# Kernel tuning notes

Hardware: AMD Instinct MI355X
Metric: run time of the kernel (lower is better)

The kernel has to match this reference:

```python
import jax, jax.numpy as jnp
import numpy as np

QLEN, BSZ, D_MODEL = 2048, 4, 1024
N_HEAD, D_HEAD = 16, 64
SCALE = 1.0 / D_HEAD ** 0.5


def _rope(t, cos, sin):
    # t: [len, b, n, d_head]; cos/sin: [len, d_head//2]
    tr = t.reshape(*t.shape[:-1], D_HEAD // 2, 2)
    t_r, t_i = tr[..., 0], tr[..., 1]
    c = cos[:, None, None, :]
    s = sin[:, None, None, :]
    o_r = t_r * c - t_i * s
    o_i = t_r * s + t_i * c
    return jnp.stack([o_r, o_i], axis=-1).reshape(t.shape)


def setup_inputs() -> dict:
    key = jax.random.key(0)
    ks = jax.random.split(key, 9)
    x = jax.random.normal(ks[0], (QLEN, BSZ, D_MODEL), dtype=jnp.float32)
    # standard RoPE frequencies: theta = 10000^{-2i/d_head}
    inv_freq = 1.0 / (10000.0 ** (np.arange(0, D_HEAD, 2, dtype=np.float32) / D_HEAD))
    ang = np.arange(QLEN, dtype=np.float32)[:, None] * inv_freq[None, :]
    freqs_cos = jnp.asarray(np.cos(ang))
    freqs_sin = jnp.asarray(np.sin(ang))
    init = lambda k, sh: (jax.random.normal(k, sh, dtype=jnp.float32) * 0.02)
    H = N_HEAD * D_HEAD
    return {
        "x": x,
        "freqs_cos": freqs_cos,
        "freqs_sin": freqs_sin,
        "Wq": init(ks[1], (D_MODEL, H)), "bq": jnp.zeros((H,), jnp.float32),
        "Wk": init(ks[2], (D_MODEL, H)), "bk": jnp.zeros((H,), jnp.float32),
        "Wv": init(ks[3], (D_MODEL, H)), "bv": jnp.zeros((H,), jnp.float32),
        "Wo": init(ks[4], (H, D_MODEL)), "bo": jnp.zeros((D_MODEL,), jnp.float32),
    }


def reference(x, freqs_cos, freqs_sin, Wq, bq, Wk, bk, Wv, bv, Wo, bo):
    qlen, bsz, _ = x.shape
    q = x @ Wq + bq  # [q, b, n*d]
    k = x @ Wk + bk
    v = x @ Wv + bv
    new_mem = (k, v)
    q = q.reshape(qlen, bsz, N_HEAD, D_HEAD)
    k = k.reshape(qlen, bsz, N_HEAD, D_HEAD)
    vv = v.reshape(qlen, bsz, N_HEAD, D_HEAD)
    q = _rope(q, freqs_cos, freqs_sin)
    k = _rope(k, freqs_cos, freqs_sin)
    attn = jnp.einsum('ibnd,jbnd->ijbn', q, k) * SCALE
    p = jax.nn.softmax(attn, axis=1)
    o = jnp.einsum('ijbn,jbnd->ibnd', p, vv)
    o = o.reshape(qlen, bsz, N_HEAD * D_HEAD) @ Wo + bo
    return (o, new_mem[0], new_mem[1])
```

## Files before the change

### kernel.cpp

```cpp
#include <hip/hip_runtime.h>

typedef __attribute__((ext_vector_type(2))) float f32x2;
typedef __attribute__((ext_vector_type(4))) float f32x4;
typedef __attribute__((ext_vector_type(16))) float f32x16;
typedef __attribute__((ext_vector_type(8))) __bf16 bf16x8;
typedef __attribute__((ext_vector_type(4))) __bf16 bf16x4;
typedef __attribute__((ext_vector_type(2))) __bf16 bf16x2;
typedef __attribute__((ext_vector_type(4))) unsigned int u32x4;

#define DEVI __device__ __forceinline__

static constexpr int QLEN = 2048, BSZ = 4, DM = 1024, NH = 16, DH = 64;
static constexpr int MROWS = QLEN * BSZ;
static constexpr long OSZ  = (long)MROWS * DM;
static constexpr float SCL2E = 0.125f * 1.4426950408889634f;

DEVI void gload_lds16(const void* g, void* l) {
  __builtin_amdgcn_global_load_lds(
      (__attribute__((address_space(1))) void*)(size_t)g,
      (__attribute__((address_space(3))) void*)l, 16, 0, 0);
}

DEVI f32x16 zero16() {
  f32x16 v;
#pragma unroll
  for (int i = 0; i < 16; ++i) v[i] = 0.f;
  return v;
}

DEVI unsigned pack_bf16(float lo, float hi) {
  bf16x2 v = { (__bf16)lo, (__bf16)hi };
  return __builtin_bit_cast(unsigned, v);
}

struct f2x8 { f32x2 h[8]; };

DEVI f32x2 pk_add(f32x2 a, f32x2 b) {
  f32x2 d;
  asm("v_pk_add_f32 %0, %1, %2" : "=v"(d) : "v"(a), "v"(b));
  return d;
}

__global__ void k_f32_to_bf16(const float* __restrict__ in, __bf16* __restrict__ out, int n4) {
  int i = blockIdx.x * blockDim.x + threadIdx.x;
  int stride = gridDim.x * blockDim.x;
  for (; i < n4; i += stride) {
    const float4 v = ((const float4*)in)[i];
    bf16x4 o = { (__bf16)v.x, (__bf16)v.y, (__bf16)v.z, (__bf16)v.w };
    ((bf16x4*)out)[i] = o;
  }
}

__global__ void k_wtrans4(const float* __restrict__ W0, const float* __restrict__ W1,
                          const float* __restrict__ W2, const float* __restrict__ W3,
                          __bf16* __restrict__ WtAll) {
  __shared__ float tile[64][65];
  const int g = blockIdx.x >> 8;
  const float* W = g == 0 ? W0 : (g == 1 ? W1 : (g == 2 ? W2 : W3));
  __bf16* Wt = WtAll + (size_t)g * DM * DM;
  const int bid = blockIdx.x & 255;
  const int tk = bid >> 4;
  const int tn = bid & 15;
  const int t = threadIdx.x;
  const int r = t >> 4;
  const int c4 = (t & 15) << 2;
#pragma unroll
  for (int i = 0; i < 4; ++i) {
    const float4 v = *(const float4*)&W[(size_t)(tk * 64 + r + i * 16) * DM + tn * 64 + c4];
    tile[r + i * 16][c4 + 0] = v.x;
    tile[r + i * 16][c4 + 1] = v.y;
    tile[r + i * 16][c4 + 2] = v.z;
    tile[r + i * 16][c4 + 3] = v.w;
  }
  __syncthreads();
#pragma unroll
  for (int i = 0; i < 4; ++i) {
    const int n = r + i * 16;
    bf16x4 o = { (__bf16)tile[c4 + 0][n], (__bf16)tile[c4 + 1][n],
                 (__bf16)tile[c4 + 2][n], (__bf16)tile[c4 + 3][n] };
    *(bf16x4*)&Wt[(size_t)(tn * 64 + n) * DM + tk * 64 + c4] = o;
  }
}

__global__ __launch_bounds__(256, 4) void k_vtrans(const __bf16* __restrict__ vb,
                                                   __bf16* __restrict__ VT) {
  __shared__ __bf16 tile[128 * 72];
  const int t = threadIdx.x;
  const int bh = blockIdx.x >> 4;
  const int s0 = (blockIdx.x & 15) * 128;
  const int b = bh >> 4, h = bh & 15;

  {
    const int r = t >> 1, hh = t & 1;
    const __bf16* src = vb + (size_t)((s0 + r) * 4 + b) * DM + h * 64 + hh * 32;
    __bf16* dst = tile + r * 72 + hh * 32;
#pragma unroll
    for (int k = 0; k < 4; ++k)
      *(bf16x8*)(dst + k * 8) = *(const bf16x8*)(src + k * 8);
  }
  __syncthreads();

  const int l = t & 63;
  const int w = t >> 6;
  const int hf = l >> 5;
#pragma unroll
  for (int gi = 0; gi < 4; ++gi) {
    const int idx = w * 4 + gi;
    const int ktl = idx >> 3;
    const int fi = idx & 7;
    const int jc = fi >> 1, dh = fi & 1;
    const int d = dh * 32 + (l & 31);
    const int j8 = ktl * 64 + jc * 16 + hf * 8;
    bf16x8 pk;
#pragma unroll
    for (int jj = 0; jj < 8; ++jj) pk[jj] = tile[(j8 + jj) * 72 + d];
    const int kt_g = (blockIdx.x & 15) * 2 + ktl;
    *(bf16x8*)&VT[(size_t)(((bh * 32 + kt_g) * 8 + fi) * 64 + l) * 8] = pk;
  }
}

DEVI void gemm_tile_core(const __bf16* __restrict__ A, const __bf16* __restrict__ Bt,
                         char* Alds, char* Blds, int m0, int n0, int t,
                         f32x4 (&acc)[4][4]) {
  constexpr int K = 1024;
  const int l = t & 63;
  const int w = t >> 6;
  const int wr = w >> 1, wc = w & 1;

  int a_addr[2][4], b_addr[2][4];
#pragma unroll
  for (int s = 0; s < 2; ++s)
#pragma unroll
    for (int f = 0; f < 4; ++f) {
      const int ca = s * 64 + ((l >> 4) << 4);
      const int ra = wr * 64 + f * 16 + (l & 15);
      a_addr[s][f] = ra * 128 + (ca ^ ((ra & 7) << 4));
      const int rb = wc * 64 + f * 16 + (l & 15);
      b_addr[s][f] = rb * 128 + (ca ^ ((rb & 7) << 4));
    }

  int g_row[4], g_col[4];
#pragma unroll
  for (int i = 0; i < 4; ++i) {
    const int g = i * 256 + t;
    g_row[i] = g >> 3;
    g_col[i] = ((g & 7) ^ (g_row[i] & 7)) * 8;
  }

  for (int kt = 0; kt < K / 64; ++kt) {
#pragma unroll
    for (int i = 0; i < 4; ++i) {
      gload_lds16(A + (size_t)(m0 + g_row[i]) * K + kt * 64 + g_col[i],
                  Alds + (size_t)(i * 256 + t) * 16);
      gload_lds16(Bt + (size_t)(n0 + g_row[i]) * K + kt * 64 + g_col[i],
                  Blds + (size_t)(i * 256 + t) * 16);
    }
    __syncthreads();
#pragma unroll
    for (int s = 0; s < 2; ++s) {
      bf16x8 af[4], bfr[4];
#pragma unroll
      for (int f = 0; f < 4; ++f) {
        af[f]  = *(const bf16x8*)(Alds + a_addr[s][f]);
        bfr[f] = *(const bf16x8*)(Blds + b_addr[s][f]);
      }
      __builtin_amdgcn_s_setprio(1);
#pragma unroll
      for (int mi = 0; mi < 4; ++mi)
#pragma unroll
        for (int ni = 0; ni < 4; ++ni)
          acc[mi][ni] = __builtin_amdgcn_mfma_f32_16x16x32_bf16(af[mi], bfr[ni], acc[mi][ni], 0, 0, 0);
      __builtin_amdgcn_s_setprio(0);
    }
    __syncthreads();
  }
}

__global__ __launch_bounds__(256, 3) void k_gemm(
    const __bf16* __restrict__ A, const __bf16* __restrict__ Bt,
    const float* __restrict__ bias, float* __restrict__ Cf) {
  __shared__ alignas(16) char lds[32768];
  const int t = threadIdx.x;
  const int l = t & 63;
  const int w = t >> 6;
  const int n0 = (blockIdx.x & 7) * 128;
  const int m0 = (blockIdx.x >> 3) * 128;
  const int wr = w >> 1, wc = w & 1;

  f32x4 acc[4][4];
#pragma unroll
  for (int i = 0; i < 4; ++i)
#pragma unroll
    for (int j = 0; j < 4; ++j) acc[i][j] = (f32x4){0.f, 0.f, 0.f, 0.f};

  gemm_tile_core(A, Bt, lds, lds + 16384, m0, n0, t, acc);

  const int rowb = m0 + wr * 64 + ((l >> 4) << 2);
  const int colb = n0 + wc * 64 + (l & 15);
#pragma unroll
  for (int ni = 0; ni < 4; ++ni) {
    const float bv = bias[colb + ni * 16];
#pragma unroll
    for (int mi = 0; mi < 4; ++mi)
#pragma unroll
      for (int r = 0; r < 4; ++r)
        Cf[(size_t)(rowb + mi * 16 + r) * 1024 + colb + ni * 16] = acc[mi][ni][r] + bv;
  }
}

__global__ __launch_bounds__(256, 3) void k_gemm_qkv(
    const __bf16* __restrict__ A, const __bf16* __restrict__ Bt,
    const float* __restrict__ bq, const float* __restrict__ bk, const float* __restrict__ bv,
    const float* __restrict__ fc, const float* __restrict__ fs,
    float* __restrict__ ok, float* __restrict__ ov,
    __bf16* __restrict__ qr, __bf16* __restrict__ kr, __bf16* __restrict__ vb) {
  __shared__ alignas(16) char lds[32768];
  const int t = threadIdx.x;
  const int l = t & 63;
  const int w = t >> 6;
  const int nt = blockIdx.x % 24;
  const int n0 = nt * 128;
  const int m0 = (blockIdx.x / 24) * 128;
  const int wr = w >> 1, wc = w & 1;

  f32x4 acc[4][4];
#pragma unroll
  for (int i = 0; i < 4; ++i)
#pragma unroll
    for (int j = 0; j < 4; ++j) acc[i][j] = (f32x4){0.f, 0.f, 0.f, 0.f};

  gemm_tile_core(A, Bt, lds, lds + 16384, m0, n0, t, acc);

  const int grp = n0 >> 10;
  const int rowb = m0 + wr * 64 + ((l >> 4) << 2);
  const int colb = (n0 & 1023) + wc * 64 + (l & 15);

  if (grp == 2) {
#pragma unroll
    for (int ni = 0; ni < 4; ++ni) {
      const float bvv = bv[colb + ni * 16];
#pragma unroll
      for (int mi = 0; mi < 4; ++mi)
#pragma unroll
        for (int r = 0; r < 4; ++r) {
          const float v = acc[mi][ni][r] + bvv;
          const size_t idx = (size_t)(rowb + mi * 16 + r) * 1024 + colb + ni * 16;
          ov[idx] = v;
          vb[idx] = (__bf16)v;
        }
    }
  } else {
    const float* bias = grp == 0 ? bq : bk;
    __bf16* Rb = grp == 0 ? qr : kr;
    const float scl = grp == 0 ? SCL2E : 1.0f;
    const float sgn = (l & 1) ? 1.f : -1.f;
#pragma unroll
    for (int ni = 0; ni < 4; ++ni) {
      const int col = colb + ni * 16;
      const float bvv = bias[col];
      const int p = (col & 63) >> 1;
#pragma unroll
      for (int mi = 0; mi < 4; ++mi) {
        const int s_idx = (rowb + mi * 16) >> 2;
        const float cv = fc[s_idx * 32 + p] * scl;
        const float sv = fs[s_idx * 32 + p] * scl * sgn;
#pragma unroll
        for (int r = 0; r < 4; ++r) {
          const float v = acc[mi][ni][r] + bvv;
          if (grp == 1) ok[(size_t)(rowb + mi * 16 + r) * 1024 + col] = v;
          const float part = __shfl_xor(v, 1);
          Rb[(size_t)(rowb + mi * 16 + r) * 1024 + col] = (__bf16)(v * cv + part * sv);
        }
      }
    }
  }
}

static constexpr int FBUF9 = 16384;

__global__ __launch_bounds__(256, 4) void k_flash9(
    const __bf16* __restrict__ Q, const __bf16* __restrict__ Kr,
    const __bf16* __restrict__ VT, __bf16* __restrict__ O) {
  __shared__ alignas(16) char lds[2 * FBUF9];

  const int t = threadIdx.x, l = t & 63, w = t >> 6;
  const int hf = l >> 5;
  const int q32 = l & 31;
  const int swz = (blockIdx.x & 7) * 128 + (blockIdx.x >> 3);
  const int qt = swz & 15;
  const int bh = swz >> 4;
  const int b = bh >> 4, hd = bh & 15;

  const int qrow = qt * 128 + w * 32 + q32;

  bf16x8 qf[4];
#pragma unroll
  for (int kc = 0; kc < 4; ++kc)
    qf[kc] = *(const bf16x8*)(Q + (size_t)(qrow * 4 + b) * DM + hd * 64 + kc * 16 + hf * 8);

  f32x16 acc0 = zero16(), acc1 = zero16();
  float l_run = 0.f;

  const size_t KSTRIDE = (size_t)64 * 4 * DM;
  const size_t VSTRIDE = (size_t)512 * 8;
  const __bf16* kp0 = Kr + (size_t)((t & 31) * 4 + b) * DM + hd * 64 + (t >> 5) * 8;
  const __bf16* kp1 = kp0 + (size_t)32 * 4 * DM;
  const __bf16* vp0 = VT + ((size_t)(bh * 32) * 512 + t) * 8;
  const __bf16* vp1 = vp0 + 256 * 8;

  char* const K0 = lds;
  char* const V0 = lds + 8192;
  char* const K1 = lds + FBUF9;
  char* const V1 = K1 + 8192;

#define STAGE9(Kn, Vn)                          \
  do {                                          \
    gload_lds16(kp0, (Kn) + t * 16);            \
    gload_lds16(kp1, (Kn) + 4096 + t * 16);     \
    gload_lds16(vp0, (Vn) + t * 16);            \
    gload_lds16(vp1, (Vn) + 4096 + t * 16);     \
    kp0 += KSTRIDE; kp1 += KSTRIDE;             \
    vp0 += VSTRIDE; vp1 += VSTRIDE;             \
  } while (0)

  auto PROCESS = [&](const char* Kl, const char* Vl) {
    f32x16 s0 = zero16(), s1 = zero16();
    __builtin_amdgcn_s_setprio(1);
#pragma unroll
    for (int kc = 0; kc < 4; ++kc) {
      const bf16x8 kf0 = *(const bf16x8*)(Kl + (0 * 4 + kc) * 1024 + l * 16);
      const bf16x8 kf1 = *(const bf16x8*)(Kl + (1 * 4 + kc) * 1024 + l * 16);
      s0 = __builtin_amdgcn_mfma_f32_32x32x16_bf16(kf0, qf[kc], s0, 0, 0, 0);
      s1 = __builtin_amdgcn_mfma_f32_32x32x16_bf16(kf1, qf[kc], s1, 0, 0, 0);
    }
    __builtin_amdgcn_s_setprio(0);

    f32x16 p0, p1;
#pragma unroll
    for (int r = 0; r < 16; ++r) {
      p0[r] = __builtin_amdgcn_exp2f(s0[r]);
      p1[r] = __builtin_amdgcn_exp2f(s1[r]);
    }

    const f2x8 P0 = __builtin_bit_cast(f2x8, p0);
    const f2x8 P1 = __builtin_bit_cast(f2x8, p1);
    f32x2 a8[8];
#pragma unroll
    for (int j = 0; j < 8; ++j) a8[j] = pk_add(P0.h[j], P1.h[j]);
#pragma unroll
    for (int j = 0; j < 4; ++j) a8[j] = pk_add(a8[j], a8[j + 4]);
    a8[0] = pk_add(a8[0], a8[2]);
    a8[1] = pk_add(a8[1], a8[3]);
    a8[0] = pk_add(a8[0], a8[1]);
    float rs = a8[0][0] + a8[0][1];
    rs += __shfl_xor(rs, 32);
    l_run += rs;

    unsigned pkw[16];
#pragma unroll
    for (int j = 0; j < 8; ++j) {
      pkw[j]     = pack_bf16(P0.h[j][0], P0.h[j][1]);
      pkw[8 + j] = pack_bf16(P1.h[j][0], P1.h[j][1]);
    }

#pragma unroll
    for (int c = 0; c < 2; ++c)
#pragma unroll
      for (int jc2 = 0; jc2 < 2; ++jc2) {
        unsigned w0 = pkw[c * 8 + 4 * jc2 + 0], w2 = pkw[c * 8 + 4 * jc2 + 2];
        unsigned w1 = pkw[c * 8 + 4 * jc2 + 1], w3 = pkw[c * 8 + 4 * jc2 + 3];
        asm("v_permlane32_swap_b32 %0, %1" : "+v"(w0), "+v"(w2));
        asm("v_permlane32_swap_b32 %0, %1" : "+v"(w1), "+v"(w3));
        const u32x4 pw = { w0, w1, w2, w3 };
        const bf16x8 pf = __builtin_bit_cast(bf16x8, pw);
        const int jc = c * 2 + jc2;
        const bf16x8 vf0 = *(const bf16x8*)(Vl + (jc * 2 + 0) * 1024 + l * 16);
        const bf16x8 vf1 = *(const bf16x8*)(Vl + (jc * 2 + 1) * 1024 + l * 16);
        __builtin_amdgcn_s_setprio(1);
        acc0 = __builtin_amdgcn_mfma_f32_32x32x16_bf16(vf0, pf, acc0, 0, 0, 0);
        acc1 = __builtin_amdgcn_mfma_f32_32x32x16_bf16(vf1, pf, acc1, 0, 0, 0);
        __builtin_amdgcn_s_setprio(0);
      }
  };

  STAGE9(K0, V0);

  for (int kt = 0; kt < QLEN / 64; kt += 2) {
    __syncthreads();
    STAGE9(K1, V1);
    PROCESS(K0, V0);
    __syncthreads();
    if (kt + 2 < QLEN / 64) STAGE9(K0, V0);
    PROCESS(K1, V1);
  }
#undef STAGE9

  const float inv = 1.0f / l_run;
#pragma unroll
  for (int g = 0; g < 4; ++g) {
    {
      const int d0 = 8 * g + 4 * hf;
      bf16x4 o4 = { (__bf16)(acc0[4 * g + 0] * inv), (__bf16)(acc0[4 * g + 1] * inv),
                    (__bf16)(acc0[4 * g + 2] * inv), (__bf16)(acc0[4 * g + 3] * inv) };
      *(bf16x4*)&O[(size_t)(qrow * 4 + b) * DM + hd * 64 + d0] = o4;
    }
    {
      const int d0 = 32 + 8 * g + 4 * hf;
      bf16x4 o4 = { (__bf16)(acc1[4 * g + 0] * inv), (__bf16)(acc1[4 * g + 1] * inv),
                    (__bf16)(acc1[4 * g + 2] * inv), (__bf16)(acc1[4 * g + 3] * inv) };
      *(bf16x4*)&O[(size_t)(qrow * 4 + b) * DM + hd * 64 + d0] = o4;
    }
  }
}

extern "C" void kernel_launch(void* const* d_in, const int* in_sizes, int n_in,
                              void* d_out, int out_size, void* d_ws, size_t ws_size,
                              hipStream_t stream) {
  const float* x    = (const float*)d_in[0];
  const float* fcos = (const float*)d_in[1];
  const float* fsin = (const float*)d_in[2];
  const float* Wq   = (const float*)d_in[3];
  const float* bq   = (const float*)d_in[4];
  const float* Wk   = (const float*)d_in[5];
  const float* bk   = (const float*)d_in[6];
  const float* Wv   = (const float*)d_in[7];
  const float* bv   = (const float*)d_in[8];
  const float* Wo   = (const float*)d_in[9];
  const float* bo   = (const float*)d_in[10];

  float* out_o = (float*)d_out;
  float* out_k = out_o + OSZ;
  float* out_v = out_o + 2 * OSZ;

  char* ws = (char*)d_ws;
  __bf16* xb  = (__bf16*)(ws);
  __bf16* VT  = (__bf16*)(ws);
  __bf16* wqt = (__bf16*)(ws + 16777216);
  __bf16* wot = (__bf16*)(ws + 23068672);
  __bf16* qr  = (__bf16*)(ws + 25165824);
  __bf16* kr  = (__bf16*)(ws + 41943040);
  __bf16* vb  = (__bf16*)(ws + 58720256);
  __bf16* ao  = (__bf16*)(ws + 75497472);

  k_f32_to_bf16<<<2048, 256, 0, stream>>>(x, xb, (int)(OSZ / 4));
  k_wtrans4<<<1024, 256, 0, stream>>>(Wq, Wk, Wv, Wo, wqt);

  k_gemm_qkv<<<1536, 256, 0, stream>>>(xb, wqt, bq, bk, bv, fcos, fsin,
                                       out_k, out_v, qr, kr, vb);

  k_vtrans<<<1024, 256, 0, stream>>>(vb, VT);

  k_flash9<<<1024, 256, 0, stream>>>(qr, kr, VT, ao);

  k_gemm<<<512, 256, 0, stream>>>(ao, wot, bo, out_o);
}
```

Before: 198.4 us.

## Merge prep kernels, raise occupancy bounds, peel first QK MFMA, use permlane swap

Merges the x-to-bf16 conversion and the four weight transposes into one launch to save a kernel launch and its tail. Raises the launch_bounds occupancy hint on both GEMMs (3→4) and on the flash kernel (4→5), which may force register spills. In the flash kernel, the first QK MFMA is peeled to accumulate from a constant zero instead of zeroing the accumulators first. The cross-half row-sum shuffle is replaced with a v_permlane32_swap.

After: 264.8 us. 33.4% more time.

```diff
diff --git a/kernel.cpp b/kernel.cpp
--- a/kernel.cpp
+++ b/kernel.cpp
@@ -41,44 +41,45 @@
   return d;
 }
 
-__global__ void k_f32_to_bf16(const float* __restrict__ in, __bf16* __restrict__ out, int n4) {
-  int i = blockIdx.x * blockDim.x + threadIdx.x;
-  int stride = gridDim.x * blockDim.x;
-  for (; i < n4; i += stride) {
-    const float4 v = ((const float4*)in)[i];
-    bf16x4 o = { (__bf16)v.x, (__bf16)v.y, (__bf16)v.z, (__bf16)v.w };
-    ((bf16x4*)out)[i] = o;
-  }
-}
-
-__global__ void k_wtrans4(const float* __restrict__ W0, const float* __restrict__ W1,
-                          const float* __restrict__ W2, const float* __restrict__ W3,
-                          __bf16* __restrict__ WtAll) {
+__global__ void k_prep(const float* __restrict__ x, __bf16* __restrict__ xb,
+                       const float* __restrict__ W0, const float* __restrict__ W1,
+                       const float* __restrict__ W2, const float* __restrict__ W3,
+                       __bf16* __restrict__ WtAll) {
   __shared__ float tile[64][65];
-  const int g = blockIdx.x >> 8;
-  const float* W = g == 0 ? W0 : (g == 1 ? W1 : (g == 2 ? W2 : W3));
-  __bf16* Wt = WtAll + (size_t)g * DM * DM;
-  const int bid = blockIdx.x & 255;
-  const int tk = bid >> 4;
-  const int tn = bid & 15;
   const int t = threadIdx.x;
-  const int r = t >> 4;
-  const int c4 = (t & 15) << 2;
-#pragma unroll
-  for (int i = 0; i < 4; ++i) {
-    const float4 v = *(const float4*)&W[(size_t)(tk * 64 + r + i * 16) * DM + tn * 64 + c4];
-    tile[r + i * 16][c4 + 0] = v.x;
-    tile[r + i * 16][c4 + 1] = v.y;
-    tile[r + i * 16][c4 + 2] = v.z;
-    tile[r + i * 16][c4 + 3] = v.w;
-  }
-  __syncthreads();
-#pragma unroll
-  for (int i = 0; i < 4; ++i) {
-    const int n = r + i * 16;
-    bf16x4 o = { (__bf16)tile[c4 + 0][n], (__bf16)tile[c4 + 1][n],
-                 (__bf16)tile[c4 + 2][n], (__bf16)tile[c4 + 3][n] };
-    *(bf16x4*)&Wt[(size_t)(tn * 64 + n) * DM + tk * 64 + c4] = o;
+  if (blockIdx.x < 1024) {
+    const int g = blockIdx.x >> 8;
+    const float* W = g == 0 ? W0 : (g == 1 ? W1 : (g == 2 ? W2 : W3));
+    __bf16* Wt = WtAll + (size_t)g * DM * DM;
+    const int bid = blockIdx.x & 255;
+    const int tk = bid >> 4;
+    const int tn = bid & 15;
+    const int r = t >> 4;
+    const int c4 = (t & 15) << 2;
+#pragma unroll
+    for (int i = 0; i < 4; ++i) {
+      const float4 v = *(const float4*)&W[(size_t)(tk * 64 + r + i * 16) * DM + tn * 64 + c4];
+      tile[r + i * 16][c4 + 0] = v.x;
+      tile[r + i * 16][c4 + 1] = v.y;
+      tile[r + i * 16][c4 + 2] = v.z;
+      tile[r + i * 16][c4 + 3] = v.w;
+    }
+    __syncthreads();
+#pragma unroll
+    for (int i = 0; i < 4; ++i) {
+      const int n = r + i * 16;
+      bf16x4 o = { (__bf16)tile[c4 + 0][n], (__bf16)tile[c4 + 1][n],
+                   (__bf16)tile[c4 + 2][n], (__bf16)tile[c4 + 3][n] };
+      *(bf16x4*)&Wt[(size_t)(tn * 64 + n) * DM + tk * 64 + c4] = o;
+    }
+  } else {
+    const int n4 = (int)(OSZ / 4);
+    int i = (blockIdx.x - 1024) * 256 + t;
+    for (; i < n4; i += 2048 * 256) {
+      const float4 v = ((const float4*)x)[i];
+      bf16x4 o = { (__bf16)v.x, (__bf16)v.y, (__bf16)v.z, (__bf16)v.w };
+      ((bf16x4*)xb)[i] = o;
+    }
   }
 }
 
@@ -176,7 +177,7 @@
   }
 }
 
-__global__ __launch_bounds__(256, 3) void k_gemm(
+__global__ __launch_bounds__(256, 4) void k_gemm(
     const __bf16* __restrict__ A, const __bf16* __restrict__ Bt,
     const float* __restrict__ bias, float* __restrict__ Cf) {
   __shared__ alignas(16) char lds[32768];
@@ -208,7 +209,7 @@
   }
 }
 
-__global__ __launch_bounds__(256, 3) void k_gemm_qkv(
+__global__ __launch_bounds__(256, 4) void k_gemm_qkv(
     const __bf16* __restrict__ A, const __bf16* __restrict__ Bt,
     const float* __restrict__ bq, const float* __restrict__ bk, const float* __restrict__ bv,
     const float* __restrict__ fc, const float* __restrict__ fs,
@@ -276,12 +277,12 @@
   }
 }
 
-static constexpr int FBUF9 = 16384;
-
-__global__ __launch_bounds__(256, 4) void k_flash9(
+static constexpr int FBUF10 = 16384;
+
+__global__ __launch_bounds__(256, 5) void k_flash10(
     const __bf16* __restrict__ Q, const __bf16* __restrict__ Kr,
     const __bf16* __restrict__ VT, __bf16* __restrict__ O) {
-  __shared__ alignas(16) char lds[2 * FBUF9];
+  __shared__ alignas(16) char lds[2 * FBUF10];
 
   const int t = threadIdx.x, l = t & 63, w = t >> 6;
   const int hf = l >> 5;
@@ -298,6 +299,7 @@
   for (int kc = 0; kc < 4; ++kc)
     qf[kc] = *(const bf16x8*)(Q + (size_t)(qrow * 4 + b) * DM + hd * 64 + kc * 16 + hf * 8);
 
+  const f32x16 Z = zero16();
   f32x16 acc0 = zero16(), acc1 = zero16();
   float l_run = 0.f;
 
@@ -310,10 +312,10 @@
 
   char* const K0 = lds;
   char* const V0 = lds + 8192;
-  char* const K1 = lds + FBUF9;
+  char* const K1 = lds + FBUF10;
   char* const V1 = K1 + 8192;
 
-#define STAGE9(Kn, Vn)                          \
+#define STAGE10(Kn, Vn)                         \
   do {                                          \
     gload_lds16(kp0, (Kn) + t * 16);            \
     gload_lds16(kp1, (Kn) + 4096 + t * 16);     \
@@ -324,10 +326,13 @@
   } while (0)
 
   auto PROCESS = [&](const char* Kl, const char* Vl) {
-    f32x16 s0 = zero16(), s1 = zero16();
+    const bf16x8 kf00 = *(const bf16x8*)(Kl + 0 * 1024 + l * 16);
+    const bf16x8 kf10 = *(const bf16x8*)(Kl + 4 * 1024 + l * 16);
     __builtin_amdgcn_s_setprio(1);
-#pragma unroll
-    for (int kc = 0; kc < 4; ++kc) {
+    f32x16 s0 = __builtin_amdgcn_mfma_f32_32x32x16_bf16(kf00, qf[0], Z, 0, 0, 0);
+    f32x16 s1 = __builtin_amdgcn_mfma_f32_32x32x16_bf16(kf10, qf[0], Z, 0, 0, 0);
+#pragma unroll
+    for (int kc = 1; kc < 4; ++kc) {
       const bf16x8 kf0 = *(const bf16x8*)(Kl + (0 * 4 + kc) * 1024 + l * 16);
       const bf16x8 kf1 = *(const bf16x8*)(Kl + (1 * 4 + kc) * 1024 + l * 16);
       s0 = __builtin_amdgcn_mfma_f32_32x32x16_bf16(kf0, qf[kc], s0, 0, 0, 0);
@@ -353,7 +358,11 @@
     a8[1] = pk_add(a8[1], a8[3]);
     a8[0] = pk_add(a8[0], a8[1]);
     float rs = a8[0][0] + a8[0][1];
-    rs += __shfl_xor(rs, 32);
+    {
+      float tmp = rs;
+      asm("v_permlane32_swap_b32 %0, %1" : "+v"(rs), "+v"(tmp));
+      rs = rs + tmp;
+    }
     l_run += rs;
 
     unsigned pkw[16];
@@ -383,17 +392,17 @@
       }
   };
 
-  STAGE9(K0, V0);
+  STAGE10(K0, V0);
 
   for (int kt = 0; kt < QLEN / 64; kt += 2) {
     __syncthreads();
-    STAGE9(K1, V1);
+    STAGE10(K1, V1);
     PROCESS(K0, V0);
     __syncthreads();
-    if (kt + 2 < QLEN / 64) STAGE9(K0, V0);
+    if (kt + 2 < QLEN / 64) STAGE10(K0, V0);
     PROCESS(K1, V1);
   }
-#undef STAGE9
+#undef STAGE10
 
   const float inv = 1.0f / l_run;
 #pragma unroll
@@ -442,15 +451,14 @@
   __bf16* vb  = (__bf16*)(ws + 58720256);
   __bf16* ao  = (__bf16*)(ws + 75497472);
 
-  k_f32_to_bf16<<<2048, 256, 0, stream>>>(x, xb, (int)(OSZ / 4));
-  k_wtrans4<<<1024, 256, 0, stream>>>(Wq, Wk, Wv, Wo, wqt);
+  k_prep<<<3072, 256, 0, stream>>>(x, xb, Wq, Wk, Wv, Wo, wqt);
 
   k_gemm_qkv<<<1536, 256, 0, stream>>>(xb, wqt, bq, bk, bv, fcos, fsin,
                                        out_k, out_v, qr, kr, vb);
 
   k_vtrans<<<1024, 256, 0, stream>>>(vb, VT);
 
-  k_flash9<<<1024, 256, 0, stream>>>(qr, kr, VT, ao);
+  k_flash10<<<1024, 256, 0, stream>>>(qr, kr, VT, ao);
 
   k_gemm<<<512, 256, 0, stream>>>(ao, wot, bo, out_o);
 }
```
